# Kernel tuning notes

Hardware: AMD Instinct MI355X
Metric: run time of the kernel (lower is better)

## Reference

```python
import jax, jax.numpy as jnp
import numpy as np

N_STATES = 64   # n_dice
N_OBS = 128     # number of distinct roll values (rows of log_likelihood table)
T = 262144      # sequence length


def setup_inputs() -> dict:
    key = jax.random.key(0)
    k1, k2, k3 = jax.random.split(key, 3)
    rolls = jax.random.randint(k1, (T,), 0, N_OBS)
    # torch.nn.init.normal(param, -1, 0.1): mean -1, std 0.1
    transition = jax.random.normal(k2, (N_STATES, N_STATES + 1), dtype=jnp.float32) * 0.1 - 1.0
    # emission log-likelihood table [n_obs, n_states]
    loglik_table = jax.nn.log_softmax(
        jax.random.normal(k3, (N_OBS, N_STATES), dtype=jnp.float32), axis=0)
    return {"rolls": rolls, "transition": transition, "loglik_table": loglik_table}


def reference(rolls, transition, loglik_table):
    """Viterbi decode: returns (path, final_score).

    Faithful to CRF.forward / _viterbi_algorithm, including the quirk that the
    emission vector ll_t is added along the PREVIOUS-state axis
    (roll.view(1,-1) broadcast over prev states), and that the returned path is
    in reverse-time order [s_{T-1}, ..., s_0].
    """
    S = transition.shape[0]
    ll = loglik_table[rolls]                 # [T, S]
    trans = transition[:, :S]                # [S, S]  (next, prev)
    init_delta = transition[:, S] + ll[0]    # [S]     start scores

    def step(delta, ll_t):
        # scores[next, prev] = trans[next, prev] + ll_t[prev] + delta[prev]
        scores = trans + (ll_t + delta)[None, :]
        bp = jnp.argmax(scores, axis=1)      # [S] backpointers
        return jnp.max(scores, axis=1), bp

    final_delta, bps = jax.lax.scan(step, init_delta, ll[1:])  # bps: [T-1, S]
    final_state = jnp.argmax(final_delta)
    final_score = final_delta[final_state]

    def back(state, bp_t):
        prev = bp_t[state]
        return prev, prev

    # reverse-time backtrack; ys[t] = decoded state at time t (t = 0..T-2)
    _, ys = jax.lax.scan(back, final_state, bps, reverse=True)
    path = jnp.concatenate([final_state[None], ys[::-1]])  # [s_{T-1},...,s_0]
    return path, final_score
```

## Files before the change

kernel.cpp:

```cpp
#include <hip/hip_runtime.h>
#include <hip/hip_fp16.h>
#include <stdint.h>

#define T_LEN 262144
#define S 64
#define SP1 65

#define L_FWD 32
#define W_FWD 4
#define C_FWD (T_LEN / L_FWD)

#define LB2 8
#define VB2 8
#define NW (T_LEN / LB2)
#define PITCH (LB2 + 2)

template <int CTRL>
__device__ __forceinline__ float dpp_fmax_step(float v) {
    int t = __builtin_amdgcn_update_dpp(__float_as_int(v), __float_as_int(v),
                                        CTRL, 0xf, 0xf, false);
    return fmaxf(__int_as_float(t), v);
}

__device__ __forceinline__ float readlane_f(float v, int lane) {
    return __int_as_float(__builtin_amdgcn_readlane(__float_as_int(v), lane));
}

__device__ __forceinline__ unsigned int pack_key(float a, int j) {
    return (__float_as_uint(a) & 0xFFFFFFC0u) | (unsigned)j;
}

__global__ __launch_bounds__(256, 8) void k1_forward(
    const int* __restrict__ rolls, const float* __restrict__ trans,
    const float* __restrict__ ll,
    unsigned int* __restrict__ bp4, int* __restrict__ wsFinal,
    float* __restrict__ out_score) {
    __shared__ __half strans_h[S * S];
    __shared__ float srowmin[S];
    __shared__ float sMc[S];
    const int tid = threadIdx.x;
    const int lane = tid & 63;
    const int wv = tid >> 6;

    if (blockIdx.x == 0 && tid == 0)
        out_score[0] = 0.0f;

    for (int k = tid; k < S * S; k += 256)
        strans_h[k] = __float2half(trans[(k & 63) * SP1 + (k >> 6)]);
    __syncthreads();

    {
        int i = tid >> 2, q = tid & 3;
        float mn = 3.0e38f;
        #pragma unroll
        for (int u = 0; u < 16; ++u)
            mn = fminf(mn, __half2float(strans_h[((q * 16 + u) << 6) | i]));
        mn = fminf(mn, __shfl_xor(mn, 1));
        mn = fminf(mn, __shfl_xor(mn, 2));
        if (q == 0) srowmin[i] = mn;
    }
    __syncthreads();
    {
        int j = tid >> 2, q = tid & 3;
        float mc = 3.0e38f;
        #pragma unroll
        for (int u = 0; u < 16; ++u) {
            int i = q * 16 + u;
            mc = fminf(mc, srowmin[i] - __half2float(strans_h[(j << 6) | i]));
        }
        mc = fminf(mc, __shfl_xor(mc, 1));
        mc = fminf(mc, __shfl_xor(mc, 2));
        if (q == 0) sMc[j] = mc;
    }
    __syncthreads();
    const float mcol = sMc[lane];

    const int c = blockIdx.x * 4 + wv;
    const int beg_out = c * L_FWD;
    int t0 = beg_out - W_FWD;
    if (t0 < 1) t0 = 1;

    int vroll = rolls[min(t0 + lane, T_LEN - 1)];

    float delta;
    if (c == 0) {
        delta = trans[lane * SP1 + S] + ll[rolls[0] * S + lane];
    } else {
        delta = 0.0f;
    }

    int r0 = __builtin_amdgcn_readlane(vroll, 0);
    int r1 = __builtin_amdgcn_readlane(vroll, 1);
    float ll_cur = ll[r0 * S + lane];
    float ll_nxt = ll[r1 * S + lane];

    int idx = 0;

    auto step = [&]() -> unsigned int {
        int rp = __builtin_amdgcn_readlane(vroll, idx + 2);
        float ll_new = ll[rp * S + lane];

        float cvec = delta + ll_cur;

        float mxc = cvec;
        mxc = dpp_fmax_step<0x111>(mxc);
        mxc = dpp_fmax_step<0x112>(mxc);
        mxc = dpp_fmax_step<0x114>(mxc);
        mxc = dpp_fmax_step<0x118>(mxc);
        mxc = dpp_fmax_step<0x142>(mxc);
        mxc = dpp_fmax_step<0x143>(mxc);
        float cmax = readlane_f(mxc, 63);

        float thr = cmax + mcol;
        unsigned long long mask = __ballot(cvec >= thr);

        int j0 = __ffsll(mask) - 1;
        unsigned long long rm = mask & (mask - 1);
        int j1 = rm ? (__ffsll(rm) - 1) : j0;
        float a0 = __half2float(strans_h[(j0 << 6) | lane]) + readlane_f(cvec, j0);
        float a1 = __half2float(strans_h[(j1 << 6) | lane]) + readlane_f(cvec, j1);
        unsigned int m = min(pack_key(a0, j0), pack_key(a1, j1));

        unsigned long long rest = rm ? (rm & (rm - 1)) : 0ull;
        if (rest) {
            int j2 = __ffsll(rest) - 1;
            unsigned long long r3 = rest & (rest - 1);
            int j3 = r3 ? (__ffsll(r3) - 1) : j2;
            float a2 = __half2float(strans_h[(j2 << 6) | lane]) + readlane_f(cvec, j2);
            float a3 = __half2float(strans_h[(j3 << 6) | lane]) + readlane_f(cvec, j3);
            m = min(m, min(pack_key(a2, j2), pack_key(a3, j3)));
            rest = r3 ? (r3 & (r3 - 1)) : 0ull;
            while (rest) {
                int j = __ffsll(rest) - 1;
                rest &= (rest - 1);
                float a = __half2float(strans_h[(j << 6) | lane]) + readlane_f(cvec, j);
                m = min(m, pack_key(a, j));
            }
        }

        delta = __uint_as_float(m & 0xFFFFFFC0u);
        ll_cur = ll_nxt;
        ll_nxt = ll_new;
        ++idx;
        return m;
    };

    if (c != 0) {
        #pragma unroll
        for (int w = 0; w < W_FWD; ++w)
            (void)step();
    }

    const int qb = beg_out >> 2;
    unsigned int pk[8];
    {
        unsigned int p = 0u;
        int u0 = (c == 0) ? 1 : 0;
        for (int u = u0; u < 4; ++u) {
            unsigned int m = step();
            p = (p >> 8) | ((m & 63u) << 24);
        }
        pk[0] = p;
    }
    #pragma unroll
    for (int q = 1; q < 8; ++q) {
        unsigned int p = 0u;
        #pragma unroll
        for (int u = 0; u < 4; ++u) {
            unsigned int m = step();
            p = (p >> 8) | ((m & 63u) << 24);
        }
        pk[q] = p;
    }
    #pragma unroll
    for (int q = 0; q < 8; ++q)
        bp4[(unsigned)((qb + q) << 6) | (unsigned)lane] = pk[q];

    if (c == C_FWD - 1) {
        float fmx = delta;
        for (int off = 32; off; off >>= 1)
            fmx = fmaxf(fmx, __shfl_xor(fmx, off));
        unsigned long long em = __ballot(delta == fmx);
        if (lane == 0)
            *wsFinal = __ffsll(em) - 1;
    }
}

__global__ __launch_bounds__(256) void k2_backtrack(
    const unsigned int* __restrict__ bp4, const int* __restrict__ wsFinal,
    const int* __restrict__ rolls, const float* __restrict__ trans,
    const float* __restrict__ ll, float* __restrict__ out_path,
    float* __restrict__ out_score) {
    __shared__ int sst[256 * PITCH];
    __shared__ float spart[4];
    const int tid = threadIdx.x;
    const int b = blockIdx.x * 256 + tid;
    const int tlo = b * LB2;
    const int thi = tlo + LB2 - 1;
    int te = thi + VB2;
    int s;
    if (te >= T_LEN - 1) {
        te = T_LEN - 1;
        s = *wsFinal;
    } else {
        s = 0;
    }
    int* row = sst + tid * PITCH;
    #pragma unroll
    for (int u = 0; u < LB2 + VB2 - 1; ++u) {
        int t = te - u;
        if (t > tlo) {
            if (t <= thi + 1) row[t - tlo] = s;
            unsigned int w = bp4[((unsigned)(t >> 2) << 6) | (unsigned)s];
            s = (int)((w >> ((t & 3) << 3)) & 63u);
        }
    }
    row[0] = s;
    __syncthreads();

    #pragma unroll
    for (int u = 0; u < LB2; ++u)
        out_path[T_LEN - 1 - (tlo + u)] = (float)row[u];

    float acc = 0.0f;
    #pragma unroll
    for (int u = 1; u <= LB2; ++u) {
        int t = tlo + u;
        if (t <= T_LEN - 1) {
            int sp = row[u - 1];
            int st = (u == LB2)
                         ? ((tid < 255) ? sst[(tid + 1) * PITCH] : row[LB2])
                         : row[u];
            acc += trans[st * SP1 + sp] + ll[rolls[t] * S + sp];
        }
    }
    if (b == 0) {
        int s0 = row[0];
        acc += trans[s0 * SP1 + S] + ll[rolls[0] * S + s0];
    }

    for (int off = 32; off; off >>= 1)
        acc += __shfl_xor(acc, off);
    if ((tid & 63) == 0) spart[tid >> 6] = acc;
    __syncthreads();
    if (tid == 0)
        atomicAdd(out_score, (spart[0] + spart[1]) + (spart[2] + spart[3]));
}

extern "C" void kernel_launch(void* const* d_in, const int* in_sizes, int n_in,
                              void* d_out, int out_size, void* d_ws, size_t ws_size,
                              hipStream_t stream) {
    const int* rolls = (const int*)d_in[0];
    const float* trans = (const float*)d_in[1];
    const float* ll = (const float*)d_in[2];
    float* out = (float*)d_out;
    char* ws = (char*)d_ws;
    int* wsFinal = (int*)(ws + 8);
    unsigned int* bp4 = (unsigned int*)(ws + 2048);

    k1_forward<<<C_FWD / 4, 256, 0, stream>>>(rolls, trans, ll, bp4, wsFinal,
                                              out + T_LEN);
    k2_backtrack<<<NW / 256, 256, 0, stream>>>(bp4, wsFinal, rolls, trans, ll,
                                               out, out + T_LEN);
}
```

Before: 109.7 us.

## Cache emission table in LDS, double chunk length, compute bounds in registers

Copies the full 128x64 log-likelihood table into shared memory so each step's emission lookup is an LDS read instead of a global gather, dropping the register prefetch pipeline. Doubles the forward chunk length to halve the relative warm-up overhead and reads rolls for two 64-lane windows. Replaces the shared-memory row/column-min reductions with per-lane register loops and readlane, and widens the pruning threshold by a small epsilon. Occupancy hint drops to 4 blocks per CU and LDS use grows to about 40KB per block, and the pk loop is no longer force-unrolled so the pk array may spill.

```diff
diff --git a/kernel.cpp b/kernel.cpp
--- a/kernel.cpp
+++ b/kernel.cpp
@@ -6,7 +6,7 @@
 #define S 64
 #define SP1 65
 
-#define L_FWD 32
+#define L_FWD 64
 #define W_FWD 4
 #define C_FWD (T_LEN / L_FWD)
 
@@ -30,14 +30,13 @@
     return (__float_as_uint(a) & 0xFFFFFFC0u) | (unsigned)j;
 }
 
-__global__ __launch_bounds__(256, 8) void k1_forward(
+__global__ __launch_bounds__(256, 4) void k1_forward(
     const int* __restrict__ rolls, const float* __restrict__ trans,
     const float* __restrict__ ll,
     unsigned int* __restrict__ bp4, int* __restrict__ wsFinal,
     float* __restrict__ out_score) {
     __shared__ __half strans_h[S * S];
-    __shared__ float srowmin[S];
-    __shared__ float sMc[S];
+    __shared__ float sll[128 * S];
     const int tid = threadIdx.x;
     const int lane = tid & 63;
     const int wv = tid >> 6;
@@ -45,42 +44,30 @@
     if (blockIdx.x == 0 && tid == 0)
         out_score[0] = 0.0f;
 
-    for (int k = tid; k < S * S; k += 256)
-        strans_h[k] = __float2half(trans[(k & 63) * SP1 + (k >> 6)]);
+    float rm = 3.0e38f;
+    #pragma unroll
+    for (int w = 0; w < S; ++w) {
+        float v = trans[lane * SP1 + w];
+        rm = fminf(rm, v);
+        strans_h[(w << 6) | lane] = __float2half(v);
+    }
+    float mc = 3.0e38f;
+    #pragma unroll
+    for (int i = 0; i < S; ++i)
+        mc = fminf(mc, readlane_f(rm, i) - trans[i * SP1 + lane]);
+    const float mcol = mc - 0.002f;
+
+    for (int k = tid; k < 128 * S; k += 256)
+        sll[k] = ll[k];
     __syncthreads();
-
-    {
-        int i = tid >> 2, q = tid & 3;
-        float mn = 3.0e38f;
-        #pragma unroll
-        for (int u = 0; u < 16; ++u)
-            mn = fminf(mn, __half2float(strans_h[((q * 16 + u) << 6) | i]));
-        mn = fminf(mn, __shfl_xor(mn, 1));
-        mn = fminf(mn, __shfl_xor(mn, 2));
-        if (q == 0) srowmin[i] = mn;
-    }
-    __syncthreads();
-    {
-        int j = tid >> 2, q = tid & 3;
-        float mc = 3.0e38f;
-        #pragma unroll
-        for (int u = 0; u < 16; ++u) {
-            int i = q * 16 + u;
-            mc = fminf(mc, srowmin[i] - __half2float(strans_h[(j << 6) | i]));
-        }
-        mc = fminf(mc, __shfl_xor(mc, 1));
-        mc = fminf(mc, __shfl_xor(mc, 2));
-        if (q == 0) sMc[j] = mc;
-    }
-    __syncthreads();
-    const float mcol = sMc[lane];
 
     const int c = blockIdx.x * 4 + wv;
     const int beg_out = c * L_FWD;
     int t0 = beg_out - W_FWD;
     if (t0 < 1) t0 = 1;
 
-    int vroll = rolls[min(t0 + lane, T_LEN - 1)];
+    int vroll0 = rolls[min(t0 + lane, T_LEN - 1)];
+    int vroll1 = rolls[min(t0 + 64 + lane, T_LEN - 1)];
 
     float delta;
     if (c == 0) {
@@ -89,16 +76,15 @@
         delta = 0.0f;
     }
 
-    int r0 = __builtin_amdgcn_readlane(vroll, 0);
-    int r1 = __builtin_amdgcn_readlane(vroll, 1);
-    float ll_cur = ll[r0 * S + lane];
-    float ll_nxt = ll[r1 * S + lane];
-
     int idx = 0;
+    auto rollat = [&](int i) -> int {
+        return (i < 64) ? __builtin_amdgcn_readlane(vroll0, i)
+                        : __builtin_amdgcn_readlane(vroll1, i - 64);
+    };
+    float ll_cur = sll[(rollat(0) << 6) | lane];
 
     auto step = [&]() -> unsigned int {
-        int rp = __builtin_amdgcn_readlane(vroll, idx + 2);
-        float ll_new = ll[rp * S + lane];
+        float ll_nxt = sll[(rollat(idx + 1) << 6) | lane];
 
         float cvec = delta + ll_cur;
 
@@ -115,13 +101,13 @@
         unsigned long long mask = __ballot(cvec >= thr);
 
         int j0 = __ffsll(mask) - 1;
-        unsigned long long rm = mask & (mask - 1);
-        int j1 = rm ? (__ffsll(rm) - 1) : j0;
+        unsigned long long rmk = mask & (mask - 1);
+        int j1 = rmk ? (__ffsll(rmk) - 1) : j0;
         float a0 = __half2float(strans_h[(j0 << 6) | lane]) + readlane_f(cvec, j0);
         float a1 = __half2float(strans_h[(j1 << 6) | lane]) + readlane_f(cvec, j1);
         unsigned int m = min(pack_key(a0, j0), pack_key(a1, j1));
 
-        unsigned long long rest = rm ? (rm & (rm - 1)) : 0ull;
+        unsigned long long rest = rmk ? (rmk & (rmk - 1)) : 0ull;
         if (rest) {
             int j2 = __ffsll(rest) - 1;
             unsigned long long r3 = rest & (rest - 1);
@@ -140,7 +126,6 @@
 
         delta = __uint_as_float(m & 0xFFFFFFC0u);
         ll_cur = ll_nxt;
-        ll_nxt = ll_new;
         ++idx;
         return m;
     };
@@ -152,7 +137,7 @@
     }
 
     const int qb = beg_out >> 2;
-    unsigned int pk[8];
+    unsigned int pk[16];
     {
         unsigned int p = 0u;
         int u0 = (c == 0) ? 1 : 0;
@@ -162,8 +147,7 @@
         }
         pk[0] = p;
     }
-    #pragma unroll
-    for (int q = 1; q < 8; ++q) {
+    for (int q = 1; q < 16; ++q) {
         unsigned int p = 0u;
         #pragma unroll
         for (int u = 0; u < 4; ++u) {
@@ -173,7 +157,7 @@
         pk[q] = p;
     }
     #pragma unroll
-    for (int q = 0; q < 8; ++q)
+    for (int q = 0; q < 16; ++q)
         bp4[(unsigned)((qb + q) << 6) | (unsigned)lane] = pk[q];
 
     if (c == C_FWD - 1) {
```

Measured after the change: 118.7 us. +8.3%, slower.
